# Performance work log

Hardware: AMD Instinct MI355X
Metric: run time of the kernel (lower is better)

## Reference

```python
import math
import jax, jax.numpy as jnp
import numpy as np

NUM_HEADS = 16
INPUT_DIM = 1024
VALUES_DIM = 1024
HEAD_DIM = INPUT_DIM // NUM_HEADS


def _pos_embeddings(length, dim):
    # TENER positional encoding for `length` positions centered at 0: [length, dim]
    half = dim // 2
    position = jnp.arange(-(length // 2), length // 2, dtype=jnp.float32)[:, None]
    div_term = jnp.exp(jnp.arange(half, dtype=jnp.float32) * (-math.log(10000.0) / (half - 1)))
    ang = position * div_term[None, :]
    return jnp.concatenate([jnp.sin(ang), jnp.cos(ang)], axis=1)


def _shift(t):
    # [B,H,S,2S] -> [B,H,S,S] relative-position shift trick
    B, H, S, _ = t.shape
    t = jnp.concatenate([t, jnp.zeros((B, H, S, 1), t.dtype)], axis=-1)  # [B,H,S,2S+1]
    t = t.reshape(B, H, 2 * S + 1, S)[:, :, :-1].reshape(B, H, S, 2 * S)
    return t[..., S:]


def setup_inputs() -> dict:
    key = jax.random.key(0)
    ks = jax.random.split(key, 9)
    B, S, D, Dv = 2, 1024, INPUT_DIM, VALUES_DIM
    s = 1.0 / math.sqrt(D)
    return {
        "query": jax.random.normal(ks[0], (B, S, D), jnp.float32),
        "key": jax.random.normal(ks[1], (B, S, D), jnp.float32),
        "value": jax.random.normal(ks[2], (B, S, D), jnp.float32),
        "mask": jnp.ones((B, S), jnp.int32),
        "Wq": jax.random.normal(ks[3], (D, D), jnp.float32) * s,
        "bq": jnp.zeros((D,), jnp.float32),
        "Wv": jax.random.normal(ks[4], (Dv, D), jnp.float32) * s,
        "bv": jnp.zeros((Dv,), jnp.float32),
        "Wo": jax.random.normal(ks[5], (D, Dv), jnp.float32) * (1.0 / math.sqrt(Dv)),
        "bo": jnp.zeros((D,), jnp.float32),
        "v_bias": jax.random.normal(ks[6], (NUM_HEADS, HEAD_DIM), jnp.float32) * (1.0 / math.sqrt(HEAD_DIM)),
    }


def reference(query, key, value, mask, Wq, bq, Wv, bv, Wo, bo, v_bias):
    B, S, D = query.shape
    H, d = NUM_HEADS, HEAD_DIM
    dv = VALUES_DIM // H
    pos = _pos_embeddings(2 * S, d)  # [2S, d]

    k = key.reshape(B, S, H, d).transpose(0, 2, 1, 3)                       # [B,H,S,d] (no projection!)
    q = (query @ Wq.T + bq).reshape(B, S, H, d).transpose(0, 2, 1, 3)       # [B,H,S,d]
    v = (value @ Wv.T + bv).reshape(B, S, H, dv).transpose(0, 2, 1, 3)      # [B,H,S,dv]

    qk = jnp.einsum('bhqd,bhkd->bhqk', q, k)                                # [B,H,S,S]
    v_bias_rel = jnp.einsum('hd,ld->hl', v_bias, pos)[None, :, None, :]     # [1,H,1,2S]
    q_rel = jnp.einsum('bhqd,ld->bhql', q, pos)                             # [B,H,S,2S]
    rel = _shift(q_rel + v_bias_rel)                                        # [B,H,S,S]

    attn = jax.nn.softmax(qk + rel, axis=-1)                                # unscaled, unmasked (matches source)
    x = jnp.einsum('bhqk,bhkd->bhqd', attn, v)                              # [B,H,S,dv]
    x = x.transpose(0, 2, 1, 3).reshape(B, S, VALUES_DIM)
    return x @ Wo.T + bo
```

## Files before the change

### kernel.cpp

```cpp
#include <hip/hip_runtime.h>
#include <math.h>

#define SEQ 1024
#define DIM 1024
#define NH 16
#define HD 64
#define NB 2

typedef __attribute__((ext_vector_type(8))) short bf16x8;
typedef __attribute__((ext_vector_type(4))) float f32x4;
typedef __attribute__((ext_vector_type(8))) unsigned short ushort8;
typedef __attribute__((ext_vector_type(4))) unsigned short ushort4v;

#define DT_CONST (-0.2971077539347156f)
#define FIXEDM 32.0f

__device__ __forceinline__ unsigned short f2bf(float x) {
    unsigned u = __float_as_uint(x);
    return (unsigned short)((u + 0x7fffu + ((u >> 16) & 1u)) >> 16);
}
__device__ __forceinline__ float bf2f(unsigned short h) {
    return __uint_as_float(((unsigned)h) << 16);
}
__device__ __forceinline__ void bfsplit(float x, unsigned short& hi, unsigned short& lo) {
    hi = f2bf(x);
    lo = f2bf(x - bf2f(hi));
}

__device__ __forceinline__ void split8(const float* __restrict__ s,
                                       unsigned short* __restrict__ h,
                                       unsigned short* __restrict__ l, int i) {
    float4 v0 = *(const float4*)&s[i];
    float4 v1 = *(const float4*)&s[i + 4];
    float vs[8] = {v0.x, v0.y, v0.z, v0.w, v1.x, v1.y, v1.z, v1.w};
    ushort8 hv, lv;
    #pragma unroll
    for (int k = 0; k < 8; ++k) {
        unsigned short hi, lo;
        bfsplit(vs[k], hi, lo);
        hv[k] = hi; lv[k] = lo;
    }
    *(ushort8*)&h[i] = hv;
    *(ushort8*)&l[i] = lv;
}
__device__ __forceinline__ void plain8(const float* __restrict__ s,
                                       unsigned short* __restrict__ h, int i) {
    float4 v0 = *(const float4*)&s[i];
    float4 v1 = *(const float4*)&s[i + 4];
    float vs[8] = {v0.x, v0.y, v0.z, v0.w, v1.x, v1.y, v1.z, v1.w};
    ushort8 hv;
    #pragma unroll
    for (int k = 0; k < 8; ++k) hv[k] = f2bf(vs[k]);
    *(ushort8*)&h[i] = hv;
}

__global__ __launch_bounds__(256) void conv_all(
    const float* __restrict__ query, const float* __restrict__ key,
    const float* __restrict__ value, const float* __restrict__ Wq,
    const float* __restrict__ Wv, const float* __restrict__ Wo,
    unsigned short* __restrict__ Aqh, unsigned short* __restrict__ Aql,
    unsigned short* __restrict__ Khs,
    unsigned short* __restrict__ Vb,
    unsigned short* __restrict__ Wqh, unsigned short* __restrict__ Wql,
    unsigned short* __restrict__ Wvh, unsigned short* __restrict__ Woh,
    unsigned short* __restrict__ Kth)
{
    int i = (blockIdx.x * 256 + threadIdx.x) * 8;
    int r = blockIdx.y;
    const int NSMALL = DIM * DIM;
    if (r >= 3 && r <= 5 && i >= NSMALL) return;
    if (r == 6 && i >= SEQ * HD) return;
    switch (r) {
        case 0: split8(query, Aqh, Aql, i); break;
        case 1: plain8(key,   Khs, i); break;
        case 2: plain8(value, Vb, i); break;
        case 3: split8(Wq, Wqh, Wql, i); break;
        case 4: plain8(Wv, Wvh, i); break;
        case 5: plain8(Wo, Woh, i); break;
        case 6: {
            ushort8 hv;
            #pragma unroll
            for (int k = 0; k < 8; ++k) {
                int idx = i + k;
                int j = idx >> 6;
                int c = idx & 63;
                int ii = c & 31;
                float dt = __expf((float)ii * DT_CONST);
                float ang = (float)j * dt;
                float val = (c < 32) ? sinf(ang) : cosf(ang);
                hv[k] = f2bf(val);
            }
            *(ushort8*)&Kth[i] = hv;
            break;
        }
    }
}

#define QLD 72

__global__ __launch_bounds__(256) void qv_gemm(
    const unsigned short* __restrict__ Aqh, const unsigned short* __restrict__ Aql,
    const unsigned short* __restrict__ Wqh, const unsigned short* __restrict__ Wql,
    const float* __restrict__ bq,
    const unsigned short* __restrict__ Vb, const unsigned short* __restrict__ Wvh,
    const float* __restrict__ bv,
    const float* __restrict__ v_bias,
    unsigned short* __restrict__ Qh, unsigned short* __restrict__ Ql,
    unsigned short* __restrict__ vpT)
{
    __shared__ __align__(16) unsigned short smem[27648];
    unsigned short* sAh = smem;
    unsigned short* sAl = smem + 128 * QLD;
    unsigned short* sWh = smem + 256 * QLD;
    unsigned short* sWl = smem + 320 * QLD;

    const int K = DIM;
    bool isq = (blockIdx.z == 0);

    int tid = threadIdx.x;
    int lane = tid & 63;
    int w = tid >> 6;
    int l16 = lane & 15, quad = lane >> 4;
    int m0 = blockIdx.y * 128;
    int h = blockIdx.x;
    int n0 = h * 64;

    int ar = tid >> 2;
    int c0 = (tid & 3) << 3;
    int c1 = c0 + 32;

    const unsigned short* pAh0 = (isq ? Aqh : Vb) + (size_t)(m0 + ar) * K;
    const unsigned short* pAh1 = pAh0 + (size_t)64 * K;
    const unsigned short* pWh  = (isq ? Wqh : Wvh) + (size_t)(n0 + ar) * K;
    const unsigned short* pAl0 = Aql + (size_t)(m0 + ar) * K;
    const unsigned short* pAl1 = pAl0 + (size_t)64 * K;
    const unsigned short* pWl  = Wql + (size_t)(n0 + ar) * K;

    f32x4 acc[2][4];
    #pragma unroll
    for (int mq = 0; mq < 2; ++mq)
        #pragma unroll
        for (int nt = 0; nt < 4; ++nt)
            acc[mq][nt] = (f32x4){0.f, 0.f, 0.f, 0.f};

    ushort8 ra[4], la[4], rw[2], lw[2];
    ra[0] = *(const ushort8*)(pAh0 + c0);  ra[1] = *(const ushort8*)(pAh0 + c1);
    ra[2] = *(const ushort8*)(pAh1 + c0);  ra[3] = *(const ushort8*)(pAh1 + c1);
    rw[0] = *(const ushort8*)(pWh + c0);   rw[1] = *(const ushort8*)(pWh + c1);
    if (isq) {
        la[0] = *(const ushort8*)(pAl0 + c0);  la[1] = *(const ushort8*)(pAl0 + c1);
        la[2] = *(const ushort8*)(pAl1 + c0);  la[3] = *(const ushort8*)(pAl1 + c1);
        lw[0] = *(const ushort8*)(pWl + c0);   lw[1] = *(const ushort8*)(pWl + c1);
    }

    for (int kk = 0; kk < K; kk += 64) {
        __syncthreads();
        *(ushort8*)&sAh[ar * QLD + c0] = ra[0];
        *(ushort8*)&sAh[ar * QLD + c1] = ra[1];
        *(ushort8*)&sAh[(ar + 64) * QLD + c0] = ra[2];
        *(ushort8*)&sAh[(ar + 64) * QLD + c1] = ra[3];
        *(ushort8*)&sWh[ar * QLD + c0] = rw[0];
        *(ushort8*)&sWh[ar * QLD + c1] = rw[1];
        if (isq) {
            *(ushort8*)&sAl[ar * QLD + c0] = la[0];
            *(ushort8*)&sAl[ar * QLD + c1] = la[1];
            *(ushort8*)&sAl[(ar + 64) * QLD + c0] = la[2];
            *(ushort8*)&sAl[(ar + 64) * QLD + c1] = la[3];
            *(ushort8*)&sWl[ar * QLD + c0] = lw[0];
            *(ushort8*)&sWl[ar * QLD + c1] = lw[1];
        }
        if (kk + 64 < K) {
            int kn = kk + 64;
            ra[0] = *(const ushort8*)(pAh0 + kn + c0);  ra[1] = *(const ushort8*)(pAh0 + kn + c1);
            ra[2] = *(const ushort8*)(pAh1 + kn + c0);  ra[3] = *(const ushort8*)(pAh1 + kn + c1);
            rw[0] = *(const ushort8*)(pWh + kn + c0);   rw[1] = *(const ushort8*)(pWh + kn + c1);
            if (isq) {
                la[0] = *(const ushort8*)(pAl0 + kn + c0);  la[1] = *(const ushort8*)(pAl0 + kn + c1);
                la[2] = *(const ushort8*)(pAl1 + kn + c0);  la[3] = *(const ushort8*)(pAl1 + kn + c1);
                lw[0] = *(const ushort8*)(pWl + kn + c0);   lw[1] = *(const ushort8*)(pWl + kn + c1);
            }
        }
        __syncthreads();

        #pragma unroll
        for (int c = 0; c < 2; ++c) {
            int kpos = c * 32 + quad * 8;
            bf16x8 af[2], afl[2];
            #pragma unroll
            for (int mq = 0; mq < 2; ++mq) {
                int row = w * 32 + mq * 16 + l16;
                af[mq] = *(const bf16x8*)&sAh[row * QLD + kpos];
                if (isq) afl[mq] = *(const bf16x8*)&sAl[row * QLD + kpos];
            }
            #pragma unroll
            for (int nt = 0; nt < 4; ++nt) {
                int row = nt * 16 + l16;
                bf16x8 bh = *(const bf16x8*)&sWh[row * QLD + kpos];
                bf16x8 bl;
                if (isq) bl = *(const bf16x8*)&sWl[row * QLD + kpos];
                #pragma unroll
                for (int mq = 0; mq < 2; ++mq) {
                    acc[mq][nt] = __builtin_amdgcn_mfma_f32_16x16x32_bf16(af[mq], bh, acc[mq][nt], 0, 0, 0);
                    if (isq) {
                        acc[mq][nt] = __builtin_amdgcn_mfma_f32_16x16x32_bf16(afl[mq], bh, acc[mq][nt], 0, 0, 0);
                        acc[mq][nt] = __builtin_amdgcn_mfma_f32_16x16x32_bf16(af[mq], bl, acc[mq][nt], 0, 0, 0);
                    }
                }
            }
        }
    }

    int b = m0 >> 10;

    if (isq) {
        float bql[4], vbs[2], vbc[2], dti[2];
        #pragma unroll
        for (int nt = 0; nt < 4; ++nt) bql[nt] = bq[h * 64 + nt * 16 + l16];
        #pragma unroll
        for (int t = 0; t < 2; ++t) {
            vbs[t] = v_bias[h * 64 + t * 16 + l16];
            vbc[t] = v_bias[h * 64 + 32 + t * 16 + l16];
            dti[t] = __expf((float)(t * 16 + l16) * DT_CONST);
        }
        #pragma unroll
        for (int mq = 0; mq < 2; ++mq) {
            #pragma unroll
            for (int reg = 0; reg < 4; ++reg) {
                int row = m0 + w * 32 + mq * 16 + quad * 4 + reg;
                int q = row & (SEQ - 1);
                size_t qbase = ((size_t)(b * NH + h) * SEQ + q) * 128;
                float hv[4];
                #pragma unroll
                for (int nt = 0; nt < 4; ++nt) hv[nt] = acc[mq][nt][reg] + bql[nt];
                #pragma unroll
                for (int nt = 0; nt < 4; ++nt) {
                    unsigned short hi, lo;
                    bfsplit(hv[nt], hi, lo);
                    Qh[qbase + nt * 16 + l16] = hi;
                    Ql[qbase + nt * 16 + l16] = lo;
                }
                #pragma unroll
                for (int t = 0; t < 2; ++t) {
                    float u = hv[t] + vbs[t];
                    float wv = hv[t + 2] + vbc[t];
                    float ang = (float)q * dti[t];
                    float C = cosf(ang), S = sinf(ang);
                    float cs = u * C + wv * S;
                    float cc = wv * C - u * S;
                    unsigned short hi, lo;
                    bfsplit(cs, hi, lo);
                    Qh[qbase + 64 + t * 16 + l16] = hi;
                    Ql[qbase + 64 + t * 16 + l16] = lo;
                    bfsplit(cc, hi, lo);
                    Qh[qbase + 96 + t * 16 + l16] = hi;
                    Ql[qbase + 96 + t * 16 + l16] = lo;
                }
            }
        }
    } else {
        __syncthreads();
        unsigned short* tb = smem;
        #pragma unroll
        for (int nt = 0; nt < 4; ++nt) {
            int d = nt * 16 + l16;
            float bcol = bv[n0 + d];
            #pragma unroll
            for (int mq = 0; mq < 2; ++mq)
                #pragma unroll
                for (int reg = 0; reg < 4; ++reg) {
                    int srow = w * 32 + mq * 16 + quad * 4 + reg;
                    tb[d * 136 + srow] = f2bf(acc[mq][nt][reg] + bcol);
                }
        }
        __syncthreads();
        int s0 = m0 & (SEQ - 1);
        #pragma unroll
        for (int i = tid; i < 1024; i += 256) {
            int dd = i >> 4;
            int j16 = i & 15;
            int sb = j16 >> 3;
            int posl = (j16 & 7) << 3;
            unsigned short tmp[8];
            #pragma unroll
            for (int k = 0; k < 8; ++k) {
                int pos = posl + k;
                int sl = (pos >> 2) + (pos & 3) * 16;
                tmp[k] = tb[dd * 136 + sb * 64 + sl];
            }
            *(ushort8*)&vpT[((size_t)((b * NH + h) * 64 + dd)) * SEQ + s0 + sb * 64 + posl] =
                *(ushort8*)tmp;
        }
    }
}

__global__ __launch_bounds__(256) void out_gemm(
    const unsigned short* __restrict__ Ab, const unsigned short* __restrict__ Woh,
    const float* __restrict__ bo, float* __restrict__ C)
{
    __shared__ unsigned short sA[64][32];
    __shared__ unsigned short sW[64][32];

    const int K = DIM, N = DIM;
    int tid = threadIdx.x;
    int lane = tid & 63;
    int w = tid >> 6;
    int l16 = lane & 15, quad = lane >> 4;
    int m0 = blockIdx.y * 64, n0 = blockIdx.x * 64;

    int ar = tid >> 2, ap = (tid & 3) << 3;

    const unsigned short* pA = Ab + (size_t)(m0 + ar) * K + ap;
    const unsigned short* pW = Woh + (size_t)(n0 + ar) * K + ap;

    f32x4 acc[4];
    #pragma unroll
    for (int nt = 0; nt < 4; ++nt) acc[nt] = (f32x4){0.f, 0.f, 0.f, 0.f};

    ushort8 a0 = *(const ushort8*)pA;
    ushort8 w0 = *(const ushort8*)pW;

    for (int kk = 0; kk < K; kk += 32) {
        __syncthreads();
        *(ushort8*)&sA[ar][ap] = a0;
        *(ushort8*)&sW[ar][ap] = w0;
        if (kk + 32 < K) {
            a0 = *(const ushort8*)(pA + kk + 32);
            w0 = *(const ushort8*)(pW + kk + 32);
        }
        __syncthreads();

        bf16x8 af = *(const bf16x8*)&sA[w * 16 + l16][quad * 8];
        bf16x8 bf[4];
        #pragma unroll
        for (int nt = 0; nt < 4; ++nt)
            bf[nt] = *(const bf16x8*)&sW[nt * 16 + l16][quad * 8];
        #pragma unroll
        for (int nt = 0; nt < 4; ++nt)
            acc[nt] = __builtin_amdgcn_mfma_f32_16x16x32_bf16(af, bf[nt], acc[nt], 0, 0, 0);
    }

    #pragma unroll
    for (int nt = 0; nt < 4; ++nt) {
        int col = n0 + nt * 16 + l16;
        float bcol = bo[col];
        #pragma unroll
        for (int reg = 0; reg < 4; ++reg) {
            int row = m0 + w * 16 + quad * 4 + reg;
            C[(size_t)row * N + col] = acc[nt][reg] + bcol;
        }
    }
}

#define LDK 136
#define LDV 72

__global__ __launch_bounds__(256) void attn_mfma(
    const unsigned short* __restrict__ Kh,
    const unsigned short* __restrict__ vpT,
    const unsigned short* __restrict__ Qh,
    const unsigned short* __restrict__ Ql,
    const unsigned short* __restrict__ Kth,
    unsigned short* __restrict__ Opart,
    float* __restrict__ lsum)
{
    __shared__ unsigned short Ksh[64][LDK];
    __shared__ unsigned short Vt[64][LDV];
    __shared__ unsigned short Ps[128][LDV];

    int tid = threadIdx.x;
    int w = tid >> 6;
    int lane = tid & 63;
    int l16 = lane & 15;
    int quad = lane >> 4;

    int bid = blockIdx.x;
    int qt = bid & 7;
    int h = (bid >> 3) & 15;
    int b = (bid >> 7) & 1;
    int sp = bid >> 8;
    int q0 = qt << 7;
    int jb = sp << 3;

    int sr0 = tid >> 3, sp0 = (tid & 7) << 3;
    int sr1 = sr0 + 32;

    ushort8 pK0, pK1, pT0, pT1, pV0, pV1;
    {
        int j0 = jb << 6;
        size_t g0 = (size_t)(b * SEQ + j0 + sr0) * DIM + h * HD + sp0;
        size_t g1 = (size_t)(b * SEQ + j0 + sr1) * DIM + h * HD + sp0;
        pK0 = *(const ushort8*)&Kh[g0]; pK1 = *(const ushort8*)&Kh[g1];
        size_t t0 = (size_t)(j0 + sr0) * 64 + sp0, t1 = (size_t)(j0 + sr1) * 64 + sp0;
        pT0 = *(const ushort8*)&Kth[t0]; pT1 = *(const ushort8*)&Kth[t1];
        size_t v0 = ((size_t)((b * NH + h) * 64 + sr0)) * SEQ + j0 + sp0;
        size_t v1 = ((size_t)((b * NH + h) * 64 + sr1)) * SEQ + j0 + sp0;
        pV0 = *(const ushort8*)&vpT[v0]; pV1 = *(const ushort8*)&vpT[v1];
    }

    bf16x8 ah[2][4], al[2][4];
    #pragma unroll
    for (int phase = 0; phase < 2; ++phase) {
        const unsigned short* gsrc = (phase == 0 ? Qh : Ql);
        #pragma unroll
        for (int half = 0; half < 2; ++half) {
            const unsigned short* gq = gsrc + (((size_t)(b * NH + h)) * SEQ + q0 + half * 64) * 128;
            #pragma unroll
            for (int c = tid; c < 1024; c += 256) {
                int r = c >> 4, p = (c & 15) << 3;
                *(ushort8*)&Ksh[r][p] = *(const ushort8*)&gq[r * 128 + p];
            }
            __syncthreads();
            if ((w >> 1) == half) {
                #pragma unroll
                for (int mq = 0; mq < 2; ++mq)
                    #pragma unroll
                    for (int c = 0; c < 4; ++c) {
                        bf16x8 f = *(const bf16x8*)&Ksh[(w & 1) * 32 + mq * 16 + l16][c * 32 + quad * 8];
                        if (phase == 0) ah[mq][c] = f; else al[mq][c] = f;
                    }
            }
            __syncthreads();
        }
    }

    f32x4 oacc[2][4];
    f32x4 lacc[2];
    #pragma unroll
    for (int mq = 0; mq < 2; ++mq) {
        #pragma unroll
        for (int nb = 0; nb < 4; ++nb) oacc[mq][nb] = (f32x4){0.f, 0.f, 0.f, 0.f};
        lacc[mq] = (f32x4){0.f, 0.f, 0.f, 0.f};
    }

    bf16x8 onesv;
    #pragma unroll
    for (int k = 0; k < 8; ++k) onesv[k] = (short)0x3F80;

    for (int jt = 0; jt < 8; ++jt) {
        __syncthreads();
        *(ushort8*)&Ksh[sr0][sp0] = pK0;       *(ushort8*)&Ksh[sr1][sp0] = pK1;
        *(ushort8*)&Ksh[sr0][64 + sp0] = pT0;  *(ushort8*)&Ksh[sr1][64 + sp0] = pT1;
        *(ushort8*)&Vt[sr0][sp0] = pV0;        *(ushort8*)&Vt[sr1][sp0] = pV1;
        if (jt < 7) {
            int j0n = (jb + jt + 1) << 6;
            size_t g0 = (size_t)(b * SEQ + j0n + sr0) * DIM + h * HD + sp0;
            size_t g1 = (size_t)(b * SEQ + j0n + sr1) * DIM + h * HD + sp0;
            pK0 = *(const ushort8*)&Kh[g0]; pK1 = *(const ushort8*)&Kh[g1];
            size_t t0 = (size_t)(j0n + sr0) * 64 + sp0, t1 = (size_t)(j0n + sr1) * 64 + sp0;
            pT0 = *(const ushort8*)&Kth[t0]; pT1 = *(const ushort8*)&Kth[t1];
            size_t v0 = ((size_t)((b * NH + h) * 64 + sr0)) * SEQ + j0n + sp0;
            size_t v1 = ((size_t)((b * NH + h) * 64 + sr1)) * SEQ + j0n + sp0;
            pV0 = *(const ushort8*)&vpT[v0]; pV1 = *(const ushort8*)&vpT[v1];
        }
        __syncthreads();

        f32x4 sacc[2][4];
        #pragma unroll
        for (int mq = 0; mq < 2; ++mq)
            #pragma unroll
            for (int nb = 0; nb < 4; ++nb) sacc[mq][nb] = (f32x4){0.f, 0.f, 0.f, 0.f};
        #pragma unroll
        for (int nb = 0; nb < 4; ++nb) {
            #pragma unroll
            for (int c = 0; c < 4; ++c) {
                bf16x8 bh = *(const bf16x8*)&Ksh[nb * 16 + l16][c * 32 + quad * 8];
                #pragma unroll
                for (int mq = 0; mq < 2; ++mq) {
                    sacc[mq][nb] = __builtin_amdgcn_mfma_f32_16x16x32_bf16(ah[mq][c], bh, sacc[mq][nb], 0, 0, 0);
                    sacc[mq][nb] = __builtin_amdgcn_mfma_f32_16x16x32_bf16(al[mq][c], bh, sacc[mq][nb], 0, 0, 0);
                }
            }
        }

        #pragma unroll
        for (int mq = 0; mq < 2; ++mq) {
            #pragma unroll
            for (int r = 0; r < 4; ++r) {
                float p0 = __expf(sacc[mq][0][r] - FIXEDM);
                float p1 = __expf(sacc[mq][1][r] - FIXEDM);
                float p2 = __expf(sacc[mq][2][r] - FIXEDM);
                float p3 = __expf(sacc[mq][3][r] - FIXEDM);
                int prow = w * 32 + mq * 16 + quad * 4 + r;
                ushort4v pv4;
                pv4.x = f2bf(p0); pv4.y = f2bf(p1); pv4.z = f2bf(p2); pv4.w = f2bf(p3);
                *(ushort4v*)&Ps[prow][l16 * 4] = pv4;
            }
        }
        __syncthreads();

        #pragma unroll
        for (int kc = 0; kc < 2; ++kc) {
            bf16x8 a[2];
            #pragma unroll
            for (int mq = 0; mq < 2; ++mq) {
                a[mq] = *(const bf16x8*)&Ps[w * 32 + mq * 16 + l16][kc * 32 + quad * 8];
                lacc[mq] = __builtin_amdgcn_mfma_f32_16x16x32_bf16(a[mq], onesv, lacc[mq], 0, 0, 0);
            }
            #pragma unroll
            for (int nb = 0; nb < 4; ++nb) {
                bf16x8 bv = *(const bf16x8*)&Vt[nb * 16 + l16][kc * 32 + quad * 8];
                #pragma unroll
                for (int mq = 0; mq < 2; ++mq)
                    oacc[mq][nb] = __builtin_amdgcn_mfma_f32_16x16x32_bf16(a[mq], bv, oacc[mq][nb], 0, 0, 0);
            }
        }
    }

    const size_t OOFF = (size_t)sp * NB * NH * SEQ * 64;
    const size_t LOFF = (size_t)sp * NB * NH * SEQ;
    #pragma unroll
    for (int mq = 0; mq < 2; ++mq) {
        #pragma unroll
        for (int r = 0; r < 4; ++r) {
            int qrow = q0 + w * 32 + mq * 16 + quad * 4 + r;
            size_t rowi = (size_t)(b * NH + h) * SEQ + qrow;
            #pragma unroll
            for (int nb = 0; nb < 4; ++nb)
                Opart[OOFF + rowi * 64 + nb * 16 + l16] = f2bf(oacc[mq][nb][r]);
            if (l16 == 0)
                lsum[LOFF + rowi] = lacc[mq][r];
        }
    }
}

__global__ __launch_bounds__(256) void attn_combine(
    const unsigned short* __restrict__ Opart, const float* __restrict__ lsum,
    unsigned short* __restrict__ xab)
{
    const size_t OOFF = (size_t)NB * NH * SEQ * 64;
    const size_t LOFF = (size_t)NB * NH * SEQ;
    int tid = threadIdx.x;
    int d = tid & 63;
    size_t r = (size_t)blockIdx.x * 4 + (tid >> 6);
    int q = (int)(r & (SEQ - 1));
    int h = (int)((r >> 10) & (NH - 1));
    int b = (int)(r >> 14);

    float inv = 1.f / (lsum[r] + lsum[LOFF + r]);
    float O0 = bf2f(Opart[r * 64 + d]);
    float O1 = bf2f(Opart[OOFF + r * 64 + d]);
    float o = (O0 + O1) * inv;
    xab[((size_t)(b * SEQ + q)) * DIM + h * HD + d] = f2bf(o);
}

extern "C" void kernel_launch(void* const* d_in, const int* in_sizes, int n_in,
                              void* d_out, int out_size, void* d_ws, size_t ws_size,
                              hipStream_t stream) {
    const float* query  = (const float*)d_in[0];
    const float* key    = (const float*)d_in[1];
    const float* value  = (const float*)d_in[2];
    const float* Wq     = (const float*)d_in[4];
    const float* bq     = (const float*)d_in[5];
    const float* Wv     = (const float*)d_in[6];
    const float* bv     = (const float*)d_in[7];
    const float* Wo     = (const float*)d_in[8];
    const float* bo     = (const float*)d_in[9];
    const float* v_bias = (const float*)d_in[10];

    float* out = (float*)d_out;
    char* base = (char*)d_ws;
    const size_t MB = 1024 * 1024;

    const bool big = ws_size >= 58 * MB;

    unsigned short* Aqh = (unsigned short*)(base);
    unsigned short* Aql = (unsigned short*)(base + 4 * MB);
    unsigned short* vpT = (unsigned short*)(base + 8 * MB);
    unsigned short* Khs = (unsigned short*)(base + 12 * MB);
    unsigned short* Qh  = (unsigned short*)(base + (big ? 16 : 20) * MB);
    unsigned short* Ql  = (unsigned short*)(base + (big ? 24 : 28) * MB);
    unsigned short* Wqh = (unsigned short*)(base + (big ? 32 : 36) * MB);
    unsigned short* Wql = (unsigned short*)(base + (big ? 34 : 38) * MB);
    unsigned short* Vb  = (unsigned short*)(base + (big ? 36 : 40) * MB);
    unsigned short* Wvh = (unsigned short*)(base + (big ? 40 : 44) * MB);
    unsigned short* Woh = (unsigned short*)(base + (big ? 42 : 46) * MB);
    unsigned short* Kth = (unsigned short*)(base + (big ? 44 : 48) * MB);
    unsigned short* xab   = (unsigned short*)(base + (big ? 45 : 0) * MB);
    float*          lsum  = (float*)(base + (big ? 49 : 4) * MB);
    unsigned short* Opart = (unsigned short*)(base + (big ? 50 : 36) * MB);

    const int M = NB * SEQ;

    dim3 cgrid(M * DIM / 2048, 7);
    conv_all<<<cgrid, 256, 0, stream>>>(query, key, value, Wq, Wv, Wo,
                                        Aqh, Aql, Khs, Vb, Wqh, Wql, Wvh, Woh, Kth);

    dim3 qvgrid(NH, M / 128, 2);
    qv_gemm<<<qvgrid, 256, 0, stream>>>(Aqh, Aql, Wqh, Wql, bq, Vb, Wvh, bv,
                                        v_bias, Qh, Ql, vpT);

    attn_mfma<<<2 * NB * NH * (SEQ / 128), 256, 0, stream>>>(Khs, vpT, Qh, Ql,
                                                             Kth, Opart, lsum);

    attn_combine<<<NB * NH * SEQ / 4, 256, 0, stream>>>(Opart, lsum, xab);

    dim3 ogrid(DIM / 64, M / 64);
    out_gemm<<<ogrid, 256, 0, stream>>>(xab, Woh, bo, out);
}
```

Measured before the change: 183.6 us.

## Replace split-bf16 hi/lo Q and QK path with single fp16 MFMA

```diff
diff --git a/kernel.cpp b/kernel.cpp
--- a/kernel.cpp
+++ b/kernel.cpp
@@ -8,6 +8,7 @@
 #define NB 2
 
 typedef __attribute__((ext_vector_type(8))) short bf16x8;
+typedef __attribute__((ext_vector_type(8))) _Float16 f16x8;
 typedef __attribute__((ext_vector_type(4))) float f32x4;
 typedef __attribute__((ext_vector_type(8))) unsigned short ushort8;
 typedef __attribute__((ext_vector_type(4))) unsigned short ushort4v;
@@ -22,27 +23,11 @@
 __device__ __forceinline__ float bf2f(unsigned short h) {
     return __uint_as_float(((unsigned)h) << 16);
 }
-__device__ __forceinline__ void bfsplit(float x, unsigned short& hi, unsigned short& lo) {
-    hi = f2bf(x);
-    lo = f2bf(x - bf2f(hi));
-}
-
-__device__ __forceinline__ void split8(const float* __restrict__ s,
-                                       unsigned short* __restrict__ h,
-                                       unsigned short* __restrict__ l, int i) {
-    float4 v0 = *(const float4*)&s[i];
-    float4 v1 = *(const float4*)&s[i + 4];
-    float vs[8] = {v0.x, v0.y, v0.z, v0.w, v1.x, v1.y, v1.z, v1.w};
-    ushort8 hv, lv;
-    #pragma unroll
-    for (int k = 0; k < 8; ++k) {
-        unsigned short hi, lo;
-        bfsplit(vs[k], hi, lo);
-        hv[k] = hi; lv[k] = lo;
-    }
-    *(ushort8*)&h[i] = hv;
-    *(ushort8*)&l[i] = lv;
-}
+__device__ __forceinline__ unsigned short f2h(float x) {
+    _Float16 h = (_Float16)x;
+    return __builtin_bit_cast(unsigned short, h);
+}
+
 __device__ __forceinline__ void plain8(const float* __restrict__ s,
                                        unsigned short* __restrict__ h, int i) {
     float4 v0 = *(const float4*)&s[i];
@@ -53,16 +38,27 @@
     for (int k = 0; k < 8; ++k) hv[k] = f2bf(vs[k]);
     *(ushort8*)&h[i] = hv;
 }
+__device__ __forceinline__ void plain8h(const float* __restrict__ s,
+                                        unsigned short* __restrict__ h, int i) {
+    float4 v0 = *(const float4*)&s[i];
+    float4 v1 = *(const float4*)&s[i + 4];
+    float vs[8] = {v0.x, v0.y, v0.z, v0.w, v1.x, v1.y, v1.z, v1.w};
+    ushort8 hv;
+    #pragma unroll
+    for (int k = 0; k < 8; ++k) hv[k] = f2h(vs[k]);
+    *(ushort8*)&h[i] = hv;
+}
 
 __global__ __launch_bounds__(256) void conv_all(
     const float* __restrict__ query, const float* __restrict__ key,
     const float* __restrict__ value, const float* __restrict__ Wq,
     const float* __restrict__ Wv, const float* __restrict__ Wo,
-    unsigned short* __restrict__ Aqh, unsigned short* __restrict__ Aql,
+    unsigned short* __restrict__ Aqh,
     unsigned short* __restrict__ Khs,
     unsigned short* __restrict__ Vb,
-    unsigned short* __restrict__ Wqh, unsigned short* __restrict__ Wql,
-    unsigned short* __restrict__ Wvh, unsigned short* __restrict__ Woh,
+    unsigned short* __restrict__ Wqh,
+    unsigned short* __restrict__ Wvh,
+    unsigned short* __restrict__ Woh,
     unsigned short* __restrict__ Kth)
 {
     int i = (blockIdx.x * 256 + threadIdx.x) * 8;
@@ -71,10 +67,10 @@
     if (r >= 3 && r <= 5 && i >= NSMALL) return;
     if (r == 6 && i >= SEQ * HD) return;
     switch (r) {
-        case 0: split8(query, Aqh, Aql, i); break;
-        case 1: plain8(key,   Khs, i); break;
+        case 0: plain8h(query, Aqh, i); break;
+        case 1: plain8h(key,   Khs, i); break;
         case 2: plain8(value, Vb, i); break;
-        case 3: split8(Wq, Wqh, Wql, i); break;
+        case 3: plain8h(Wq, Wqh, i); break;
         case 4: plain8(Wv, Wvh, i); break;
         case 5: plain8(Wo, Woh, i); break;
         case 6: {
@@ -88,7 +84,7 @@
                 float dt = __expf((float)ii * DT_CONST);
                 float ang = (float)j * dt;
                 float val = (c < 32) ? sinf(ang) : cosf(ang);
-                hv[k] = f2bf(val);
+                hv[k] = f2h(val);
             }
             *(ushort8*)&Kth[i] = hv;
             break;
@@ -99,20 +95,17 @@
 #define QLD 72
 
 __global__ __launch_bounds__(256) void qv_gemm(
-    const unsigned short* __restrict__ Aqh, const unsigned short* __restrict__ Aql,
-    const unsigned short* __restrict__ Wqh, const unsigned short* __restrict__ Wql,
+    const unsigned short* __restrict__ Aqh, const unsigned short* __restrict__ Wqh,
     const float* __restrict__ bq,
     const unsigned short* __restrict__ Vb, const unsigned short* __restrict__ Wvh,
     const float* __restrict__ bv,
     const float* __restrict__ v_bias,
-    unsigned short* __restrict__ Qh, unsigned short* __restrict__ Ql,
+    unsigned short* __restrict__ Qh,
     unsigned short* __restrict__ vpT)
 {
-    __shared__ __align__(16) unsigned short smem[27648];
+    __shared__ __align__(16) unsigned short smem[192 * QLD];
     unsigned short* sAh = smem;
-    unsigned short* sAl = smem + 128 * QLD;
-    unsigned short* sWh = smem + 256 * QLD;
-    unsigned short* sWl = smem + 320 * QLD;
+    unsigned short* sWh = smem + 128 * QLD;
 
     const int K = DIM;
     bool isq = (blockIdx.z == 0);
@@ -132,9 +125,6 @@
     const unsigned short* pAh0 = (isq ? Aqh : Vb) + (size_t)(m0 + ar) * K;
     const unsigned short* pAh1 = pAh0 + (size_t)64 * K;
     const unsigned short* pWh  = (isq ? Wqh : Wvh) + (size_t)(n0 + ar) * K;
-    const unsigned short* pAl0 = Aql + (size_t)(m0 + ar) * K;
-    const unsigned short* pAl1 = pAl0 + (size_t)64 * K;
-    const unsigned short* pWl  = Wql + (size_t)(n0 + ar) * K;
 
     f32x4 acc[2][4];
     #pragma unroll
@@ -143,15 +133,10 @@
         for (int nt = 0; nt < 4; ++nt)
             acc[mq][nt] = (f32x4){0.f, 0.f, 0.f, 0.f};
 
-    ushort8 ra[4], la[4], rw[2], lw[2];
+    ushort8 ra[4], rw[2];
     ra[0] = *(const ushort8*)(pAh0 + c0);  ra[1] = *(const ushort8*)(pAh0 + c1);
     ra[2] = *(const ushort8*)(pAh1 + c0);  ra[3] = *(const ushort8*)(pAh1 + c1);
     rw[0] = *(const ushort8*)(pWh + c0);   rw[1] = *(const ushort8*)(pWh + c1);
-    if (isq) {
-        la[0] = *(const ushort8*)(pAl0 + c0);  la[1] = *(const ushort8*)(pAl0 + c1);
-        la[2] = *(const ushort8*)(pAl1 + c0);  la[3] = *(const ushort8*)(pAl1 + c1);
-        lw[0] = *(const ushort8*)(pWl + c0);   lw[1] = *(const ushort8*)(pWl + c1);
-    }
 
     for (int kk = 0; kk < K; kk += 64) {
         __syncthreads();
@@ -161,51 +146,40 @@
         *(ushort8*)&sAh[(ar + 64) * QLD + c1] = ra[3];
         *(ushort8*)&sWh[ar * QLD + c0] = rw[0];
         *(ushort8*)&sWh[ar * QLD + c1] = rw[1];
-        if (isq) {
-            *(ushort8*)&sAl[ar * QLD + c0] = la[0];
-            *(ushort8*)&sAl[ar * QLD + c1] = la[1];
-            *(ushort8*)&sAl[(ar + 64) * QLD + c0] = la[2];
-            *(ushort8*)&sAl[(ar + 64) * QLD + c1] = la[3];
-            *(ushort8*)&sWl[ar * QLD + c0] = lw[0];
-            *(ushort8*)&sWl[ar * QLD + c1] = lw[1];
-        }
         if (kk + 64 < K) {
             int kn = kk + 64;
             ra[0] = *(const ushort8*)(pAh0 + kn + c0);  ra[1] = *(const ushort8*)(pAh0 + kn + c1);
             ra[2] = *(const ushort8*)(pAh1 + kn + c0);  ra[3] = *(const ushort8*)(pAh1 + kn + c1);
             rw[0] = *(const ushort8*)(pWh + kn + c0);   rw[1] = *(const ushort8*)(pWh + kn + c1);
-            if (isq) {
-                la[0] = *(const ushort8*)(pAl0 + kn + c0);  la[1] = *(const ushort8*)(pAl0 + kn + c1);
-                la[2] = *(const ushort8*)(pAl1 + kn + c0);  la[3] = *(const ushort8*)(pAl1 + kn + c1);
-                lw[0] = *(const ushort8*)(pWl + kn + c0);   lw[1] = *(const ushort8*)(pWl + kn + c1);
-            }
         }
         __syncthreads();
 
         #pragma unroll
         for (int c = 0; c < 2; ++c) {
             int kpos = c * 32 + quad * 8;
-            bf16x8 af[2], afl[2];
-            #pragma unroll
-            for (int mq = 0; mq < 2; ++mq) {
-                int row = w * 32 + mq * 16 + l16;
-                af[mq] = *(const bf16x8*)&sAh[row * QLD + kpos];
-                if (isq) afl[mq] = *(const bf16x8*)&sAl[row * QLD + kpos];
-            }
-            #pragma unroll
-            for (int nt = 0; nt < 4; ++nt) {
-                int row = nt * 16 + l16;
-                bf16x8 bh = *(const bf16x8*)&sWh[row * QLD + kpos];
-                bf16x8 bl;
-                if (isq) bl = *(const bf16x8*)&sWl[row * QLD + kpos];
-                #pragma unroll
-                for (int mq = 0; mq < 2; ++mq) {
-                    acc[mq][nt] = __builtin_amdgcn_mfma_f32_16x16x32_bf16(af[mq], bh, acc[mq][nt], 0, 0, 0);
-                    if (isq) {
-                        acc[mq][nt] = __builtin_amdgcn_mfma_f32_16x16x32_bf16(afl[mq], bh, acc[mq][nt], 0, 0, 0);
-                        acc[mq][nt] = __builtin_amdgcn_mfma_f32_16x16x32_bf16(af[mq], bl, acc[mq][nt], 0, 0, 0);
-                    }
-                }
+            bf16x8 af[2];
+            #pragma unroll
+            for (int mq = 0; mq < 2; ++mq)
+                af[mq] = *(const bf16x8*)&sAh[(w * 32 + mq * 16 + l16) * QLD + kpos];
+            bf16x8 bhv[4];
+            #pragma unroll
+            for (int nt = 0; nt < 4; ++nt)
+                bhv[nt] = *(const bf16x8*)&sWh[(nt * 16 + l16) * QLD + kpos];
+            if (isq) {
+                #pragma unroll
+                for (int nt = 0; nt < 4; ++nt)
+                    #pragma unroll
+                    for (int mq = 0; mq < 2; ++mq)
+                        acc[mq][nt] = __builtin_amdgcn_mfma_f32_16x16x32_f16(
+                            __builtin_bit_cast(f16x8, af[mq]),
+                            __builtin_bit_cast(f16x8, bhv[nt]), acc[mq][nt], 0, 0, 0);
+            } else {
+                #pragma unroll
+                for (int nt = 0; nt < 4; ++nt)
+                    #pragma unroll
+                    for (int mq = 0; mq < 2; ++mq)
+                        acc[mq][nt] = __builtin_amdgcn_mfma_f32_16x16x32_bf16(
+                            af[mq], bhv[nt], acc[mq][nt], 0, 0, 0);
             }
         }
     }
@@ -233,12 +207,8 @@
                 #pragma unroll
                 for (int nt = 0; nt < 4; ++nt) hv[nt] = acc[mq][nt][reg] + bql[nt];
                 #pragma unroll
-                for (int nt = 0; nt < 4; ++nt) {
-                    unsigned short hi, lo;
-                    bfsplit(hv[nt], hi, lo);
-                    Qh[qbase + nt * 16 + l16] = hi;
-                    Ql[qbase + nt * 16 + l16] = lo;
-                }
+                for (int nt = 0; nt < 4; ++nt)
+                    Qh[qbase + nt * 16 + l16] = f2h(hv[nt]);
                 #pragma unroll
                 for (int t = 0; t < 2; ++t) {
                     float u = hv[t] + vbs[t];
@@ -247,13 +217,8 @@
                     float C = cosf(ang), S = sinf(ang);
                     float cs = u * C + wv * S;
                     float cc = wv * C - u * S;
-                    unsigned short hi, lo;
-                    bfsplit(cs, hi, lo);
-                    Qh[qbase + 64 + t * 16 + l16] = hi;
-                    Ql[qbase + 64 + t * 16 + l16] = lo;
-                    bfsplit(cc, hi, lo);
-                    Qh[qbase + 96 + t * 16 + l16] = hi;
-                    Ql[qbase + 96 + t * 16 + l16] = lo;
+                    Qh[qbase + 64 + t * 16 + l16] = f2h(cs);
+                    Qh[qbase + 96 + t * 16 + l16] = f2h(cc);
                 }
             }
         }
@@ -358,7 +323,6 @@
     const unsigned short* __restrict__ Kh,
     const unsigned short* __restrict__ vpT,
     const unsigned short* __restrict__ Qh,
-    const unsigned short* __restrict__ Ql,
     const unsigned short* __restrict__ Kth,
     unsigned short* __restrict__ Opart,
     float* __restrict__ lsum)
@@ -397,30 +361,24 @@
         pV0 = *(const ushort8*)&vpT[v0]; pV1 = *(const ushort8*)&vpT[v1];
     }
 
-    bf16x8 ah[2][4], al[2][4];
-    #pragma unroll
-    for (int phase = 0; phase < 2; ++phase) {
-        const unsigned short* gsrc = (phase == 0 ? Qh : Ql);
-        #pragma unroll
-        for (int half = 0; half < 2; ++half) {
-            const unsigned short* gq = gsrc + (((size_t)(b * NH + h)) * SEQ + q0 + half * 64) * 128;
-            #pragma unroll
-            for (int c = tid; c < 1024; c += 256) {
-                int r = c >> 4, p = (c & 15) << 3;
-                *(ushort8*)&Ksh[r][p] = *(const ushort8*)&gq[r * 128 + p];
-            }
-            __syncthreads();
-            if ((w >> 1) == half) {
-                #pragma unroll
-                for (int mq = 0; mq < 2; ++mq)
-                    #pragma unroll
-                    for (int c = 0; c < 4; ++c) {
-                        bf16x8 f = *(const bf16x8*)&Ksh[(w & 1) * 32 + mq * 16 + l16][c * 32 + quad * 8];
-                        if (phase == 0) ah[mq][c] = f; else al[mq][c] = f;
-                    }
-            }
-            __syncthreads();
-        }
+    bf16x8 ah[2][4];
+    #pragma unroll
+    for (int half = 0; half < 2; ++half) {
+        const unsigned short* gq = Qh + (((size_t)(b * NH + h)) * SEQ + q0 + half * 64) * 128;
+        #pragma unroll
+        for (int c = tid; c < 1024; c += 256) {
+            int r = c >> 4, p = (c & 15) << 3;
+            *(ushort8*)&Ksh[r][p] = *(const ushort8*)&gq[r * 128 + p];
+        }
+        __syncthreads();
+        if ((w >> 1) == half) {
+            #pragma unroll
+            for (int mq = 0; mq < 2; ++mq)
+                #pragma unroll
+                for (int c = 0; c < 4; ++c)
+                    ah[mq][c] = *(const bf16x8*)&Ksh[(w & 1) * 32 + mq * 16 + l16][c * 32 + quad * 8];
+        }
+        __syncthreads();
     }
 
     f32x4 oacc[2][4];
@@ -465,10 +423,10 @@
             for (int c = 0; c < 4; ++c) {
                 bf16x8 bh = *(const bf16x8*)&Ksh[nb * 16 + l16][c * 32 + quad * 8];
                 #pragma unroll
-                for (int mq = 0; mq < 2; ++mq) {
-                    sacc[mq][nb] = __builtin_amdgcn_mfma_f32_16x16x32_bf16(ah[mq][c], bh, sacc[mq][nb], 0, 0, 0);
-                    sacc[mq][nb] = __builtin_amdgcn_mfma_f32_16x16x32_bf16(al[mq][c], bh, sacc[mq][nb], 0, 0, 0);
-                }
+                for (int mq = 0; mq < 2; ++mq)
+                    sacc[mq][nb] = __builtin_amdgcn_mfma_f32_16x16x32_f16(
+                        __builtin_bit_cast(f16x8, ah[mq][c]),
+                        __builtin_bit_cast(f16x8, bh), sacc[mq][nb], 0, 0, 0);
             }
         }
 
@@ -561,35 +519,30 @@
     char* base = (char*)d_ws;
     const size_t MB = 1024 * 1024;
 
-    const bool big = ws_size >= 58 * MB;
-
-    unsigned short* Aqh = (unsigned short*)(base);
-    unsigned short* Aql = (unsigned short*)(base + 4 * MB);
-    unsigned short* vpT = (unsigned short*)(base + 8 * MB);
-    unsigned short* Khs = (unsigned short*)(base + 12 * MB);
-    unsigned short* Qh  = (unsigned short*)(base + (big ? 16 : 20) * MB);
-    unsigned short* Ql  = (unsigned short*)(base + (big ? 24 : 28) * MB);
-    unsigned short* Wqh = (unsigned short*)(base + (big ? 32 : 36) * MB);
-    unsigned short* Wql = (unsigned short*)(base + (big ? 34 : 38) * MB);
-    unsigned short* Vb  = (unsigned short*)(base + (big ? 36 : 40) * MB);
-    unsigned short* Wvh = (unsigned short*)(base + (big ? 40 : 44) * MB);
-    unsigned short* Woh = (unsigned short*)(base + (big ? 42 : 46) * MB);
-    unsigned short* Kth = (unsigned short*)(base + (big ? 44 : 48) * MB);
-    unsigned short* xab   = (unsigned short*)(base + (big ? 45 : 0) * MB);
-    float*          lsum  = (float*)(base + (big ? 49 : 4) * MB);
-    unsigned short* Opart = (unsigned short*)(base + (big ? 50 : 36) * MB);
+    unsigned short* Aqh   = (unsigned short*)(base);
+    unsigned short* vpT   = (unsigned short*)(base +  4 * MB);
+    unsigned short* Khs   = (unsigned short*)(base +  8 * MB);
+    unsigned short* Qh    = (unsigned short*)(base + 12 * MB);
+    unsigned short* Wqh   = (unsigned short*)(base + 20 * MB);
+    unsigned short* Vb    = (unsigned short*)(base + 22 * MB);
+    unsigned short* Wvh   = (unsigned short*)(base + 26 * MB);
+    unsigned short* Woh   = (unsigned short*)(base + 28 * MB);
+    unsigned short* Kth   = (unsigned short*)(base + 30 * MB);
+    unsigned short* xab   = (unsigned short*)(base + 31 * MB);
+    float*          lsum  = (float*)(base + 35 * MB);
+    unsigned short* Opart = (unsigned short*)(base + 36 * MB);
 
     const int M = NB * SEQ;
 
     dim3 cgrid(M * DIM / 2048, 7);
     conv_all<<<cgrid, 256, 0, stream>>>(query, key, value, Wq, Wv, Wo,
-                                        Aqh, Aql, Khs, Vb, Wqh, Wql, Wvh, Woh, Kth);
+                                        Aqh, Khs, Vb, Wqh, Wvh, Woh, Kth);
 
     dim3 qvgrid(NH, M / 128, 2);
-    qv_gemm<<<qvgrid, 256, 0, stream>>>(Aqh, Aql, Wqh, Wql, bq, Vb, Wvh, bv,
-                                        v_bias, Qh, Ql, vpT);
-
-    attn_mfma<<<2 * NB * NH * (SEQ / 128), 256, 0, stream>>>(Khs, vpT, Qh, Ql,
+    qv_gemm<<<qvgrid, 256, 0, stream>>>(Aqh, Wqh, bq, Vb, Wvh, bv,
+                                        v_bias, Qh, vpT);
+
+    attn_mfma<<<2 * NB * NH * (SEQ / 128), 256, 0, stream>>>(Khs, vpT, Qh,
                                                              Kth, Opart, lsum);
 
     attn_combine<<<NB * NH * SEQ / 4, 256, 0, stream>>>(Opart, lsum, xab);
```

After: 158.3 us (median of 2 runs). -13.8%, faster.
